# Kernel tuning notes

Measured on AMD Instinct MI355X. Metric: run time of the kernel, lower is better.

## Reference

```python
import math
import jax, jax.numpy as jnp
import numpy as np

CANTOR_DEPTH = 8
CANTOR_TEMPERATURE = 1.0
SEQ_LEN = 4096


def _cantor_positions(depth_max):
    positions = [np.array([0.0, 1.0])]
    for _ in range(1, depth_max):
        prev = positions[-1]
        new = []
        for i in range(len(prev) - 1):
            left = prev[i]
            right = prev[i + 1]
            third = (right - left) / 3.0
            new.append(left)
            new.append(left + third)
        new.append(prev[-1])
        positions.append(np.array(new))
    return positions


def _cantor_indices(seq_len, depth_max):
    # indices[d] = unique sorted long indices of Cantor positions at depth d
    pos = _cantor_positions(depth_max)
    out = []
    for d in range(depth_max):
        idx = np.unique((pos[d] * (seq_len - 1)).astype(np.int64))
        out.append(jnp.asarray(idx))
    return out


# number of depths actually used in the forward loop
_N_DEPTHS = min(CANTOR_DEPTH, int(math.log2(SEQ_LEN)) + 2)
# get_cantor_indices caps depth at cantor_depth - 1 implicitly via list length
CANTOR_IDX = _cantor_indices(SEQ_LEN, CANTOR_DEPTH)


def setup_inputs() -> dict:
    key0 = jax.random.key(0)
    ks = jax.random.split(key0, 4)
    B, S, D = 8, SEQ_LEN, 512
    return {
        "query": jax.random.normal(ks[0], (B, S, D), dtype=jnp.float32),
        "key": jax.random.normal(ks[1], (B, S, D), dtype=jnp.float32),
        "value": jax.random.normal(ks[2], (B, S, D), dtype=jnp.float32),
        "t": jax.random.normal(ks[3], (B,), dtype=jnp.float32),
        "scale_weights": jnp.ones((CANTOR_DEPTH,), dtype=jnp.float32),
        "scale_temperature": jnp.ones((1,), dtype=jnp.float32),
    }


def reference(query, key, value, t, scale_weights, scale_temperature):
    D = key.shape[-1]
    inv_scale = 1.0 / (math.sqrt(D) * CANTOR_TEMPERATURE)
    scale_outputs = []
    for depth in range(_N_DEPTHS):
        idx = CANTOR_IDX[depth]            # static, <= 2^depth + 1 indices
        sk = key[:, idx]                   # [B, Nd, D] gather
        sv = value[:, idx]                 # [B, Nd, D]
        scores = jnp.einsum("bqd,bkd->bqk", query, sk) * inv_scale
        attn = jax.nn.softmax(scores, axis=-1)
        scale_outputs.append(jnp.einsum("bqk,bkd->bqd", attn, sv))
    stacked = jnp.stack(scale_outputs, axis=0)  # [depths, B, Q, D]
    w = jax.nn.softmax(scale_weights[: len(scale_outputs)] / scale_temperature[0])
    out = jnp.sum(stacked * w[:, None, None, None], axis=0)  # [B, Q, D]
    # torch .squeeze(1) is a no-op here since Q != 1
    return out
```

## Files before the change

kernel.cpp:

```cpp
#include <hip/hip_runtime.h>

#define NDEPTH 8
#define NK 129
#define SEQB 4096
#define DIM 512

typedef short bf16x8 __attribute__((ext_vector_type(8)));
typedef float f32x4  __attribute__((ext_vector_type(4)));

struct CTab { int uidx[NK]; int minD[NK]; int count; };

static constexpr CTab make_ctab() {
    CTab T{};
    double pos[NDEPTH][NK] = {}; int cnt[NDEPTH] = {};
    pos[0][0] = 0.0; pos[0][1] = 1.0; cnt[0] = 2;
    for (int d = 1; d < NDEPTH; ++d) {
        const int n = cnt[d - 1]; int m = 0;
        for (int i = 0; i < n - 1; ++i) {
            const double left = pos[d - 1][i], right = pos[d - 1][i + 1];
            const double third = (right - left) / 3.0;
            pos[d][m++] = left; pos[d][m++] = left + third;
        }
        pos[d][m++] = pos[d - 1][n - 1]; cnt[d] = m;
    }
    int idx[NDEPTH][NK] = {}; int icnt[NDEPTH] = {};
    for (int d = 0; d < NDEPTH; ++d) {
        int m = 0;
        for (int i = 0; i < cnt[d]; ++i) {
            const long long v = (long long)(pos[d][i] * 4095.0);
            bool dup = false;
            for (int k = 0; k < m; ++k) if (idx[d][k] == (int)v) dup = true;
            if (!dup) idx[d][m++] = (int)v;
        }
        icnt[d] = m;
    }
    int u[2 * NK] = {}; int un = 0;
    for (int d = 0; d < NDEPTH; ++d)
        for (int i = 0; i < icnt[d]; ++i) {
            const int v = idx[d][i]; bool f = false;
            for (int k = 0; k < un; ++k) if (u[k] == v) f = true;
            if (!f && un < 2 * NK) u[un++] = v;
        }
    for (int i = 1; i < un; ++i) {
        const int key = u[i]; int k = i - 1;
        while (k >= 0 && u[k] > key) { u[k + 1] = u[k]; --k; }
        u[k + 1] = key;
    }
    T.count = un;
    for (int i = 0; i < un && i < NK; ++i) {
        T.uidx[i] = u[i];
        int md = NDEPTH;
        for (int d = 0; d < NDEPTH && md == NDEPTH; ++d)
            for (int k = 0; k < icnt[d]; ++k)
                if (idx[d][k] == u[i]) { md = d; break; }
        T.minD[i] = md;
    }
    return T;
}
static constexpr CTab h_ct = make_ctab();
static_assert(h_ct.count == NK, "cantor union size mismatch");
__device__ __constant__ CTab g_ct = h_ct;

__device__ __forceinline__ short f2bf(float f) {
    union { float f; unsigned u; } v; v.f = f;
    unsigned r = v.u + 0x7fffu + ((v.u >> 16) & 1u);
    return (short)(r >> 16);
}

__device__ __forceinline__ void gl_lds16(const void* g, void* lds) {
    __builtin_amdgcn_global_load_lds(
        (const __attribute__((address_space(1))) unsigned int*)g,
        (__attribute__((address_space(3))) unsigned int*)lds, 16, 0, 0);
}

#define WSK_ELEMS (8 * 144 * 512)

__global__ __launch_bounds__(256) void ufa_prep(
    const float* __restrict__ K, const float* __restrict__ V,
    short* __restrict__ ws)
{
    short* wsK  = ws;
    short* wsVt = ws + WSK_ELEMS;
    if (blockIdx.x < 1152) {
        const int b = blockIdx.x / 144, key = blockIdx.x % 144;
        short* dst = wsK + ((size_t)b * 144 + key) * 512;
        if (key < NK) {
            const float* src = K + ((size_t)b * SEQB + g_ct.uidx[key]) * DIM;
            for (int i = threadIdx.x; i < 512; i += 256) dst[i] = f2bf(src[i]);
        } else {
            for (int i = threadIdx.x; i < 512; i += 256) dst[i] = 0;
        }
    } else {
        __shared__ float tr[64][133];
        const int id = blockIdx.x - 1152;
        const int b = id / 8, dt = id % 8;
        const float* Vb = V + (size_t)b * SEQB * DIM;
        for (int it = 0; it < 33; ++it) {
            const int k = it * 4 + (int)threadIdx.x / 64;
            const int d = (int)threadIdx.x % 64;
            if (k < NK) tr[d][k] = Vb[(size_t)g_ct.uidx[k] * DIM + dt * 64 + d];
        }
        __syncthreads();
        short* dst = wsVt + ((size_t)b * 512 + dt * 64) * 192;
        for (int idx = threadIdx.x; idx < 64 * 192; idx += 256) {
            const int d = idx / 192, k = idx - d * 192;
            dst[(size_t)d * 192 + k] = (k < NK) ? f2bf(tr[d][k]) : (short)0;
        }
    }
}

__global__ __launch_bounds__(256, 2) void ufa_main(
    const float* __restrict__ Q, const short* __restrict__ ws,
    const float* __restrict__ SW, const float* __restrict__ ST,
    float* __restrict__ Out)
{
    __shared__ char smem[50176];
    char*  kv    = smem;
    short* c_lds = (short*)(smem + 24576);

    const short* wsK  = ws;
    const short* wsVt = ws + WSK_ELEMS;

    const int t    = (int)threadIdx.x;
    const int w    = t >> 6;
    const int lane = t & 63;
    const int m    = lane & 15;
    const int quad = lane >> 4;
    const int b    = (int)blockIdx.x >> 6;
    const int q0   = ((int)blockIdx.x & 63) * 64 + w * 16;

    float wgt[NDEPTH];
    {
        const float it = 1.0f / ST[0];
        float mx = -3.0e38f;
        #pragma unroll
        for (int d = 0; d < NDEPTH; ++d) { wgt[d] = SW[d] * it; mx = fmaxf(mx, wgt[d]); }
        float sum = 0.0f;
        #pragma unroll
        for (int d = 0; d < NDEPTH; ++d) { wgt[d] = __expf(wgt[d] - mx); sum += wgt[d]; }
        const float is = 1.0f / sum;
        #pragma unroll
        for (int d = 0; d < NDEPTH; ++d) wgt[d] *= is;
    }

    f32x4 acc[9];
    #pragma unroll
    for (int tt = 0; tt < 9; ++tt) acc[tt] = (f32x4){0.f, 0.f, 0.f, 0.f};

    const float* Qb  = Q + ((size_t)b * SEQB + q0 + m) * DIM;
    const short* wsKb = wsK + (size_t)b * 144 * 512;

    for (int c = 0; c < 8; ++c) {
        for (int g = w; g < 18; g += 4) {
            const int off  = g * 1024 + lane * 16;
            const int row  = off >> 7;
            const int slot = (off >> 4) & 7;
            const int slog = slot ^ (row & 7);
            gl_lds16(wsKb + (size_t)row * 512 + c * 64 + slog * 8, kv + g * 1024);
        }
        bf16x8 aq[2];
        #pragma unroll
        for (int ks = 0; ks < 2; ++ks) {
            const float* qp = Qb + c * 64 + ks * 32 + quad * 8;
            const float4 x = *(const float4*)qp;
            const float4 y = *(const float4*)(qp + 4);
            aq[ks][0] = f2bf(x.x); aq[ks][1] = f2bf(x.y);
            aq[ks][2] = f2bf(x.z); aq[ks][3] = f2bf(x.w);
            aq[ks][4] = f2bf(y.x); aq[ks][5] = f2bf(y.y);
            aq[ks][6] = f2bf(y.z); aq[ks][7] = f2bf(y.w);
        }
        __syncthreads();
        #pragma unroll
        for (int ks = 0; ks < 2; ++ks) {
            #pragma unroll
            for (int tt = 0; tt < 9; ++tt) {
                const int row  = tt * 16 + m;
                const int slog = (ks * 4 + quad) ^ (row & 7);
                const bf16x8 bk = *(const bf16x8*)(kv + row * 128 + slog * 16);
                acc[tt] = __builtin_amdgcn_mfma_f32_16x16x32_bf16(aq[ks], bk, acc[tt], 0, 0, 0);
            }
        }
        __syncthreads();
    }

    const float inv_scale = 0.04419417382415922f;
    int md9[9];
    #pragma unroll
    for (int tt = 0; tt < 9; ++tt) {
        const int j = tt * 16 + m;
        md9[tt] = (j < NK) ? g_ct.minD[j] : NDEPTH;
    }
    float ev[9][4], mxr[4];
    #pragma unroll
    for (int i = 0; i < 4; ++i) mxr[i] = -3.0e38f;
    #pragma unroll
    for (int tt = 0; tt < 9; ++tt) {
        const bool valid = (tt * 16 + m) < NK;
        #pragma unroll
        for (int i = 0; i < 4; ++i) {
            const float s = valid ? acc[tt][i] * inv_scale : -3.0e38f;
            ev[tt][i] = s;
            mxr[i] = fmaxf(mxr[i], s);
        }
    }
    #pragma unroll
    for (int off = 1; off < 16; off <<= 1)
        #pragma unroll
        for (int i = 0; i < 4; ++i) mxr[i] = fmaxf(mxr[i], __shfl_xor(mxr[i], off));

    float P[4][NDEPTH];
    #pragma unroll
    for (int i = 0; i < 4; ++i)
        #pragma unroll
        for (int d = 0; d < NDEPTH; ++d) P[i][d] = 0.0f;
    #pragma unroll
    for (int tt = 0; tt < 9; ++tt) {
        const int md = md9[tt];
        #pragma unroll
        for (int i = 0; i < 4; ++i) {
            const float e = __expf(ev[tt][i] - mxr[i]);
            ev[tt][i] = e;
            #pragma unroll
            for (int d = 0; d < NDEPTH; ++d) P[i][d] += (md == d) ? e : 0.0f;
        }
    }
    #pragma unroll
    for (int off = 1; off < 16; off <<= 1)
        #pragma unroll
        for (int i = 0; i < 4; ++i)
            #pragma unroll
            for (int d = 0; d < NDEPTH; ++d) P[i][d] += __shfl_xor(P[i][d], off);

    float T[4][NDEPTH];
    #pragma unroll
    for (int i = 0; i < 4; ++i) {
        float L = 0.0f, Lc[NDEPTH];
        #pragma unroll
        for (int d = 0; d < NDEPTH; ++d) { L += P[i][d]; Lc[d] = L; }
        float ta = 0.0f;
        #pragma unroll
        for (int d = NDEPTH - 1; d >= 0; --d) { ta += wgt[d] / Lc[d]; T[i][d] = ta; }
    }
    #pragma unroll
    for (int tt = 0; tt < 10; ++tt) {
        const int j = tt * 16 + m;
        #pragma unroll
        for (int i = 0; i < 4; ++i) {
            float cv = 0.0f;
            if (tt < 9 && j < NK) {
                const int md = md9[tt];
                float tv = 0.0f;
                #pragma unroll
                for (int d = 0; d < NDEPTH; ++d) tv = (md == d) ? T[i][d] : tv;
                cv = ev[tt][i] * tv;
            }
            c_lds[(w * 16 + quad * 4 + i) * 200 + j] = f2bf(cv);
        }
    }
    __syncthreads();

    bf16x8 ac[5];
    #pragma unroll
    for (int ks = 0; ks < 5; ++ks)
        ac[ks] = *(const bf16x8*)&c_lds[(w * 16 + m) * 200 + ks * 32 + quad * 8];

    const short* wsVb = wsVt + (size_t)b * 512 * 192;
    float* Ob = Out + ((size_t)b * SEQB + q0) * DIM;

    for (int c2 = 0; c2 < 8; ++c2) {
        __syncthreads();
        for (int g = w; g < 24; g += 4) {
            const int off  = g * 1024 + lane * 16;
            const int row  = off / 384;
            const int rem  = off - row * 384;
            const int slot = rem >> 4;
            const int slog = (slot & ~7) | ((slot & 7) ^ (row & 7));
            gl_lds16(wsVb + (size_t)(c2 * 64 + row) * 192 + slog * 8, kv + g * 1024);
        }
        __syncthreads();
        #pragma unroll
        for (int nt = 0; nt < 4; ++nt) {
            f32x4 o = (f32x4){0.f, 0.f, 0.f, 0.f};
            #pragma unroll
            for (int ks = 0; ks < 5; ++ks) {
                const int row  = nt * 16 + m;
                const int slot = ks * 4 + quad;
                const int slog = (slot & ~7) | ((slot & 7) ^ (row & 7));
                const bf16x8 bv = *(const bf16x8*)(kv + row * 384 + slog * 16);
                o = __builtin_amdgcn_mfma_f32_16x16x32_bf16(ac[ks], bv, o, 0, 0, 0);
            }
            const int n0 = c2 * 64 + nt * 16;
            #pragma unroll
            for (int i = 0; i < 4; ++i)
                Ob[(size_t)(quad * 4 + i) * DIM + n0 + m] = o[i];
        }
    }
}

extern "C" void kernel_launch(void* const* d_in, const int* in_sizes, int n_in,
                              void* d_out, int out_size, void* d_ws, size_t ws_size,
                              hipStream_t stream) {
    const float* Q  = (const float*)d_in[0];
    const float* K  = (const float*)d_in[1];
    const float* V  = (const float*)d_in[2];
    const float* SW = (const float*)d_in[4];
    const float* ST = (const float*)d_in[5];
    float* Out = (float*)d_out;
    short* ws  = (short*)d_ws;

    ufa_prep<<<dim3(1152 + 64), dim3(256), 0, stream>>>(K, V, ws);
    ufa_main<<<dim3(512), dim3(256), 0, stream>>>(Q, ws, SW, ST, Out);
}
```

Baseline: 212.4 us.

## Use single-wave blocks reading K/V operands directly from global memory

The main kernel now runs one 64-thread wave per 16-query tile (2048 blocks) instead of four waves sharing LDS-staged K and V tiles. The MFMA B operands are loaded directly from the bf16 workspace in global/L2, which removes the block-wide barriers and LDS staging. The V-transpose prep is split into finer 16-column chunks to give more blocks. The trade-off is that K/V tiles are no longer shared through LDS, so each wave does redundant global loads. That relies on L2 hit rates, and the loads are uncoalesced row-strided 16-byte reads.

```diff
diff --git a/kernel.cpp b/kernel.cpp
--- a/kernel.cpp
+++ b/kernel.cpp
@@ -65,12 +65,6 @@
     union { float f; unsigned u; } v; v.f = f;
     unsigned r = v.u + 0x7fffu + ((v.u >> 16) & 1u);
     return (short)(r >> 16);
-}
-
-__device__ __forceinline__ void gl_lds16(const void* g, void* lds) {
-    __builtin_amdgcn_global_load_lds(
-        (const __attribute__((address_space(1))) unsigned int*)g,
-        (__attribute__((address_space(3))) unsigned int*)lds, 16, 0, 0);
 }
 
 #define WSK_ELEMS (8 * 144 * 512)
@@ -91,43 +85,40 @@
             for (int i = threadIdx.x; i < 512; i += 256) dst[i] = 0;
         }
     } else {
-        __shared__ float tr[64][133];
+        __shared__ float tr[16][132];
         const int id = blockIdx.x - 1152;
-        const int b = id / 8, dt = id % 8;
-        const float* Vb = V + (size_t)b * SEQB * DIM;
-        for (int it = 0; it < 33; ++it) {
-            const int k = it * 4 + (int)threadIdx.x / 64;
-            const int d = (int)threadIdx.x % 64;
-            if (k < NK) tr[d][k] = Vb[(size_t)g_ct.uidx[k] * DIM + dt * 64 + d];
+        const int b = id >> 5, dc = id & 31;
+        const float* Vb = V + (size_t)b * SEQB * DIM + dc * 16;
+        const int kk = (int)threadIdx.x >> 4, d = (int)threadIdx.x & 15;
+        #pragma unroll
+        for (int it = 0; it < 9; ++it) {
+            const int k = it * 16 + kk;
+            if (k < NK) tr[d][k] = Vb[(size_t)g_ct.uidx[k] * DIM + d];
         }
         __syncthreads();
-        short* dst = wsVt + ((size_t)b * 512 + dt * 64) * 192;
-        for (int idx = threadIdx.x; idx < 64 * 192; idx += 256) {
-            const int d = idx / 192, k = idx - d * 192;
-            dst[(size_t)d * 192 + k] = (k < NK) ? f2bf(tr[d][k]) : (short)0;
-        }
-    }
-}
-
-__global__ __launch_bounds__(256, 2) void ufa_main(
+        short* dst = wsVt + ((size_t)b * 512 + dc * 16) * 192;
+        for (int idx = threadIdx.x; idx < 16 * 192; idx += 256) {
+            const int dd = idx / 192, k = idx - dd * 192;
+            dst[idx] = (k < NK) ? f2bf(tr[dd][k]) : (short)0;
+        }
+    }
+}
+
+__global__ __launch_bounds__(64, 4) void ufa_main(
     const float* __restrict__ Q, const short* __restrict__ ws,
     const float* __restrict__ SW, const float* __restrict__ ST,
     float* __restrict__ Out)
 {
-    __shared__ char smem[50176];
-    char*  kv    = smem;
-    short* c_lds = (short*)(smem + 24576);
+    __shared__ short c_lds[16 * 200];
 
     const short* wsK  = ws;
     const short* wsVt = ws + WSK_ELEMS;
 
-    const int t    = (int)threadIdx.x;
-    const int w    = t >> 6;
-    const int lane = t & 63;
+    const int lane = (int)threadIdx.x;
     const int m    = lane & 15;
     const int quad = lane >> 4;
-    const int b    = (int)blockIdx.x >> 6;
-    const int q0   = ((int)blockIdx.x & 63) * 64 + w * 16;
+    const int b    = (int)blockIdx.x >> 8;
+    const int q0   = ((int)blockIdx.x & 255) << 4;
 
     float wgt[NDEPTH];
     {
@@ -147,17 +138,11 @@
     #pragma unroll
     for (int tt = 0; tt < 9; ++tt) acc[tt] = (f32x4){0.f, 0.f, 0.f, 0.f};
 
-    const float* Qb  = Q + ((size_t)b * SEQB + q0 + m) * DIM;
-    const short* wsKb = wsK + (size_t)b * 144 * 512;
-
+    const float* Qb = Q + ((size_t)b * SEQB + q0 + m) * DIM;
+    const short* Kb = wsK + (size_t)b * 144 * 512;
+
+    #pragma unroll
     for (int c = 0; c < 8; ++c) {
-        for (int g = w; g < 18; g += 4) {
-            const int off  = g * 1024 + lane * 16;
-            const int row  = off >> 7;
-            const int slot = (off >> 4) & 7;
-            const int slog = slot ^ (row & 7);
-            gl_lds16(wsKb + (size_t)row * 512 + c * 64 + slog * 8, kv + g * 1024);
-        }
         bf16x8 aq[2];
         #pragma unroll
         for (int ks = 0; ks < 2; ++ks) {
@@ -169,18 +154,15 @@
             aq[ks][4] = f2bf(y.x); aq[ks][5] = f2bf(y.y);
             aq[ks][6] = f2bf(y.z); aq[ks][7] = f2bf(y.w);
         }
-        __syncthreads();
         #pragma unroll
         for (int ks = 0; ks < 2; ++ks) {
             #pragma unroll
             for (int tt = 0; tt < 9; ++tt) {
-                const int row  = tt * 16 + m;
-                const int slog = (ks * 4 + quad) ^ (row & 7);
-                const bf16x8 bk = *(const bf16x8*)(kv + row * 128 + slog * 16);
+                const bf16x8 bk = *(const bf16x8*)&Kb[(size_t)(tt * 16 + m) * 512
+                                                     + c * 64 + ks * 32 + quad * 8];
                 acc[tt] = __builtin_amdgcn_mfma_f32_16x16x32_bf16(aq[ks], bk, acc[tt], 0, 0, 0);
             }
         }
-        __syncthreads();
     }
 
     const float inv_scale = 0.04419417382415922f;
@@ -254,7 +236,7 @@
                 for (int d = 0; d < NDEPTH; ++d) tv = (md == d) ? T[i][d] : tv;
                 cv = ev[tt][i] * tv;
             }
-            c_lds[(w * 16 + quad * 4 + i) * 200 + j] = f2bf(cv);
+            c_lds[(quad * 4 + i) * 200 + j] = f2bf(cv);
         }
     }
     __syncthreads();
@@ -262,31 +244,20 @@
     bf16x8 ac[5];
     #pragma unroll
     for (int ks = 0; ks < 5; ++ks)
-        ac[ks] = *(const bf16x8*)&c_lds[(w * 16 + m) * 200 + ks * 32 + quad * 8];
-
-    const short* wsVb = wsVt + (size_t)b * 512 * 192;
+        ac[ks] = *(const bf16x8*)&c_lds[m * 200 + ks * 32 + quad * 8];
+
+    const short* Vtb = wsVt + (size_t)b * 512 * 192;
     float* Ob = Out + ((size_t)b * SEQB + q0) * DIM;
 
+    #pragma unroll
     for (int c2 = 0; c2 < 8; ++c2) {
-        __syncthreads();
-        for (int g = w; g < 24; g += 4) {
-            const int off  = g * 1024 + lane * 16;
-            const int row  = off / 384;
-            const int rem  = off - row * 384;
-            const int slot = rem >> 4;
-            const int slog = (slot & ~7) | ((slot & 7) ^ (row & 7));
-            gl_lds16(wsVb + (size_t)(c2 * 64 + row) * 192 + slog * 8, kv + g * 1024);
-        }
-        __syncthreads();
         #pragma unroll
         for (int nt = 0; nt < 4; ++nt) {
             f32x4 o = (f32x4){0.f, 0.f, 0.f, 0.f};
             #pragma unroll
             for (int ks = 0; ks < 5; ++ks) {
-                const int row  = nt * 16 + m;
-                const int slot = ks * 4 + quad;
-                const int slog = (slot & ~7) | ((slot & 7) ^ (row & 7));
-                const bf16x8 bv = *(const bf16x8*)(kv + row * 384 + slog * 16);
+                const bf16x8 bv = *(const bf16x8*)&Vtb[(size_t)(c2 * 64 + nt * 16 + m) * 192
+                                                       + ks * 32 + quad * 8];
                 o = __builtin_amdgcn_mfma_f32_16x16x32_bf16(ac[ks], bv, o, 0, 0, 0);
             }
             const int n0 = c2 * 64 + nt * 16;
@@ -308,6 +279,6 @@
     float* Out = (float*)d_out;
     short* ws  = (short*)d_ws;
 
-    ufa_prep<<<dim3(1152 + 64), dim3(256), 0, stream>>>(K, V, ws);
-    ufa_main<<<dim3(512), dim3(256), 0, stream>>>(Q, ws, SW, ST, Out);
-}
+    ufa_prep<<<dim3(1152 + 256), dim3(256), 0, stream>>>(K, V, ws);
+    ufa_main<<<dim3(2048), dim3(64), 0, stream>>>(Q, ws, SW, ST, Out);
+}
```

Measured after the change: 257.1 us. +21.1%, slower.
